# Kernel optimization log

Measured on AMD Instinct MI355X. Metric: run time of the kernel, lower is better.

## Reference

```python
import jax, jax.numpy as jnp
import numpy as np

B, S, T, C, Q = 8, 4096, 2048, 256, 256  # batch, ctx_steps, q_steps, context_size, query_size


def setup_inputs() -> dict:
    key = jax.random.key(0)
    k1, k2, k3, k4 = jax.random.split(key, 4)
    context = jax.random.normal(k1, (B, S, C), dtype=jnp.float32)
    query = jax.random.normal(k2, (T, B, Q), dtype=jnp.float32)
    context_mask = jax.random.randint(k3, (B, S), 0, 2).astype(bool)  # True = masked
    W = jax.random.normal(k4, (C, Q), dtype=jnp.float32)  # bilinear weights [context_size, query_size]
    return {"context": context, "query": query, "context_mask": context_mask, "W": W}


def reference(context, query, context_mask, W):
    # temp = 'auto' -> sqrt(query_size)
    temp = jnp.asarray(np.sqrt(Q), dtype=context.dtype)
    # scores[b,t,s] = (context[b,s,:] @ W) . query[t,b,:]
    scores = jnp.einsum('bsc,cq,tbq->bts', context, W, query) / temp
    neg = jnp.finfo(scores.dtype).min
    scores = jnp.where(context_mask[:, None, :], neg, scores)  # mask over ctx_steps
    attn = jax.nn.softmax(scores, axis=2)  # [B, T, S]
    # rows whose entire context is masked -> attention zeroed
    all_masked = jnp.all(context_mask, axis=1)[:, None, None]
    attn = jnp.where(all_masked, jnp.zeros((), attn.dtype), attn)
    composition = jnp.einsum('bts,bsc->btc', attn, context)  # [B, T, C]
    # module returns (attn, composition) permuted to [T, B, ...]
    return attn.transpose(1, 0, 2), composition.transpose(1, 0, 2)
```

## Files before the change

kernel.cpp:

```cpp
#include <hip/hip_runtime.h>

#define B_ 8
#define S_ 4096
#define T_ 2048
#define C_ 256
#define Q_ 256
#define NROW (T_ * B_)

typedef _Float16 f16;
typedef _Float16 f16x8 __attribute__((ext_vector_type(8)));
typedef _Float16 f16x4 __attribute__((ext_vector_type(4)));
typedef _Float16 f16x2 __attribute__((ext_vector_type(2)));
typedef float f32x4 __attribute__((ext_vector_type(4)));

#define MFMA(a, b, c) __builtin_amdgcn_mfma_f32_16x16x32_f16((a), (b), (c), 0, 0, 0)

__global__ void k_mask_mode(const unsigned char* __restrict__ mb, int* __restrict__ mode,
                            int* __restrict__ allm) {
  __shared__ int s0_, s123_;
  if (threadIdx.x == 0) { s0_ = 0; s123_ = 0; }
  __syncthreads();
  int a0 = 0, a123 = 0;
  int base = threadIdx.x * 128;
  for (int i = 0; i < 128; ++i) {
    int idx = base + i;
    int v = mb[idx];
    if (idx & 3) a123 |= v; else a0 |= v;
  }
  if (a0) atomicOr(&s0_, 1);
  if (a123) atomicOr(&s123_, 1);
  __syncthreads();
  if (threadIdx.x == 0) {
    int m;
    if (s123_ == 0 && s0_ == 0) m = 3;
    else if (s123_ == 0) m = 0;
    else if (s0_ == 0) m = 2;
    else m = 1;
    *mode = m;
  }
  if (threadIdx.x < B_) allm[threadIdx.x] = 1;
}

__global__ void k_expand_mask(const void* __restrict__ mp, const int* __restrict__ mode,
                              float* __restrict__ maskf, int* __restrict__ allm) {
  int i = blockIdx.x * 256 + threadIdx.x;
  int md = *mode;
  int m;
  if (md == 0)      m = ((const int*)mp)[i] != 0;
  else if (md == 1) m = ((const unsigned char*)mp)[i] != 0;
  else if (md == 2) m = ((const float*)mp)[i] != 0.0f;
  else              m = 0;
  maskf[i] = m ? 1.0f : 0.0f;
  if (!m) atomicAnd(&allm[i / S_], 0);
}

__global__ void k_conv_w(const float* __restrict__ W, f16* __restrict__ WT) {
  int i = blockIdx.x * 256 + threadIdx.x;
  int c = i >> 8, q = i & 255;
  WT[q * C_ + c] = (f16)W[i];
}

__global__ void k_conv_q(const float* __restrict__ q, f16* __restrict__ qT) {
  int i = blockIdx.x * 256 + threadIdx.x;
  int e = i * 4;
  int t = e / (B_ * Q_);
  int rb = e - t * (B_ * Q_);
  int b = rb >> 8;
  int qq = rb & 255;
  f32x4 v = *(const f32x4*)(q + e);
  f16x4 h; h[0] = (f16)v[0]; h[1] = (f16)v[1]; h[2] = (f16)v[2]; h[3] = (f16)v[3];
  *(f16x4*)(qT + ((size_t)(b * T_ + t)) * Q_ + qq) = h;
}

__global__ void k_transpose_ctx(const float* __restrict__ ctx, f16* __restrict__ ctxT) {
  __shared__ f16 tile[64][65];
  int s0 = blockIdx.x * 64, c0 = blockIdx.y * 64, b = blockIdx.z;
  int r = threadIdx.x >> 2;
  int cs = (threadIdx.x & 3) * 16;
  const float* src = ctx + ((size_t)(b * S_ + s0 + r)) * C_ + c0 + cs;
  f32x4 v0 = ((const f32x4*)src)[0];
  f32x4 v1 = ((const f32x4*)src)[1];
  f32x4 v2 = ((const f32x4*)src)[2];
  f32x4 v3 = ((const f32x4*)src)[3];
#pragma unroll
  for (int j = 0; j < 4; ++j) {
    tile[r][cs + j] = (f16)v0[j];
    tile[r][cs + 4 + j] = (f16)v1[j];
    tile[r][cs + 8 + j] = (f16)v2[j];
    tile[r][cs + 12 + j] = (f16)v3[j];
  }
  __syncthreads();
  int c = threadIdx.x >> 2;
  int ss = (threadIdx.x & 3) * 16;
  f16x8 o0, o1;
#pragma unroll
  for (int j = 0; j < 8; ++j) { o0[j] = tile[ss + j][c]; o1[j] = tile[ss + 8 + j][c]; }
  f16* dst = ctxT + ((size_t)(b * C_ + c0 + c)) * S_ + s0 + ss;
  *(f16x8*)dst = o0;
  *(f16x8*)(dst + 8) = o1;
}

__launch_bounds__(256, 2)
__global__ void k_gemm_cw(const float* __restrict__ ctx, const f16* __restrict__ WT,
                          f16* __restrict__ CW) {
  __shared__ alignas(16) f16 As[128 * 32];
  __shared__ alignas(16) f16 Bs[128 * 32];
  int n0 = blockIdx.x * 128;
  int m0 = blockIdx.y * 128;
  int tid = threadIdx.x;
  int w = tid >> 6, l = tid & 63;
  int wm = (w >> 1) * 64, wn = (w & 1) * 64;
  int lr = l & 15, lk = (l >> 4) * 8;
  f32x4 acc[4][4] = {};
  for (int k0 = 0; k0 < C_; k0 += 32) {
    __syncthreads();
#pragma unroll
    for (int it = 0; it < 2; ++it) {
      int h = (it * 256 + tid) * 8;
      int row = h >> 5, kk = h & 31;
      const float* ap = ctx + (size_t)(m0 + row) * C_ + k0 + kk;
      f32x4 x0 = ((const f32x4*)ap)[0];
      f32x4 x1 = ((const f32x4*)ap)[1];
      f16x8 hv;
#pragma unroll
      for (int j = 0; j < 4; ++j) { hv[j] = (f16)x0[j]; hv[4 + j] = (f16)x1[j]; }
      *(f16x8*)&As[row * 32 + kk] = hv;
    }
#pragma unroll
    for (int it = 0; it < 2; ++it) {
      int h = (it * 256 + tid) * 8;
      int row = h >> 5, kk = h & 31;
      *(f16x8*)&Bs[row * 32 + kk] = *(const f16x8*)&WT[(size_t)(n0 + row) * C_ + k0 + kk];
    }
    __syncthreads();
    f16x8 af[4], bf[4];
#pragma unroll
    for (int m = 0; m < 4; ++m) af[m] = *(const f16x8*)&As[(wm + m * 16 + lr) * 32 + lk];
#pragma unroll
    for (int n = 0; n < 4; ++n) bf[n] = *(const f16x8*)&Bs[(wn + n * 16 + lr) * 32 + lk];
#pragma unroll
    for (int m = 0; m < 4; ++m)
#pragma unroll
      for (int n = 0; n < 4; ++n) acc[m][n] = MFMA(af[m], bf[n], acc[m][n]);
  }
#pragma unroll
  for (int m = 0; m < 4; ++m)
#pragma unroll
    for (int n = 0; n < 4; ++n)
#pragma unroll
      for (int i = 0; i < 4; ++i) {
        int gm = m0 + wm + m * 16 + (l >> 4) * 4 + i;
        int gn = n0 + wn + n * 16 + lr;
        CW[(size_t)gm * Q_ + gn] = (f16)(acc[m][n][i] * 0.0625f);
      }
}

__launch_bounds__(256, 2)
__global__ void k_gemm_scores(const f16* __restrict__ qT, const f16* __restrict__ CW,
                              const float* __restrict__ maskf, float* __restrict__ attn,
                              float* __restrict__ pmax, float* __restrict__ psum) {
  __shared__ alignas(16) f16 As[128 * 32];
  __shared__ alignas(16) f16 Bs[128 * 32];
  int n0 = blockIdx.x * 128;
  int m0 = blockIdx.y * 128;
  int b = blockIdx.z;
  const f16* A = qT + (size_t)b * T_ * Q_;
  const f16* Bm = CW + (size_t)b * S_ * Q_;
  int tid = threadIdx.x;
  int w = tid >> 6, l = tid & 63;
  int wm = (w >> 1) * 64, wn = (w & 1) * 64;
  int lr = l & 15, lk = (l >> 4) * 8;
  f32x4 acc[4][4] = {};
  for (int k0 = 0; k0 < Q_; k0 += 32) {
    __syncthreads();
#pragma unroll
    for (int it = 0; it < 2; ++it) {
      int h = (it * 256 + tid) * 8;
      int row = h >> 5, kk = h & 31;
      *(f16x8*)&As[row * 32 + kk] = *(const f16x8*)&A[(size_t)(m0 + row) * Q_ + k0 + kk];
    }
#pragma unroll
    for (int it = 0; it < 2; ++it) {
      int h = (it * 256 + tid) * 8;
      int row = h >> 5, kk = h & 31;
      *(f16x8*)&Bs[row * 32 + kk] = *(const f16x8*)&Bm[(size_t)(n0 + row) * Q_ + k0 + kk];
    }
    __syncthreads();
    f16x8 af[4], bf[4];
#pragma unroll
    for (int m = 0; m < 4; ++m) af[m] = *(const f16x8*)&As[(wm + m * 16 + lr) * 32 + lk];
#pragma unroll
    for (int n = 0; n < 4; ++n) bf[n] = *(const f16x8*)&Bs[(wn + n * 16 + lr) * 32 + lk];
#pragma unroll
    for (int m = 0; m < 4; ++m)
#pragma unroll
      for (int n = 0; n < 4; ++n) acc[m][n] = MFMA(af[m], bf[n], acc[m][n]);
  }
  float msk[4];
#pragma unroll
  for (int n = 0; n < 4; ++n) msk[n] = maskf[b * S_ + n0 + wn + n * 16 + lr];
#pragma unroll
  for (int m = 0; m < 4; ++m)
#pragma unroll
    for (int n = 0; n < 4; ++n) {
      int gn = n0 + wn + n * 16 + lr;
#pragma unroll
      for (int i = 0; i < 4; ++i) {
        int gt = m0 + wm + m * 16 + (l >> 4) * 4 + i;
        float v = acc[m][n][i];
        if (msk[n] != 0.0f) v = -3.4e38f;
        acc[m][n][i] = v;
        attn[((size_t)gt * B_ + b) * S_ + gn] = v;
      }
    }
  int g = l >> 4;
  int ch = blockIdx.x * 2 + (w & 1);
#pragma unroll
  for (int m = 0; m < 4; ++m)
#pragma unroll
    for (int i = 0; i < 4; ++i) {
      float mx = fmaxf(fmaxf(acc[m][0][i], acc[m][1][i]), fmaxf(acc[m][2][i], acc[m][3][i]));
      mx = fmaxf(mx, __shfl_xor(mx, 1));
      mx = fmaxf(mx, __shfl_xor(mx, 2));
      mx = fmaxf(mx, __shfl_xor(mx, 4));
      mx = fmaxf(mx, __shfl_xor(mx, 8));
      float sm = 0.0f;
#pragma unroll
      for (int n = 0; n < 4; ++n) sm += __expf(acc[m][n][i] - mx);
      sm += __shfl_xor(sm, 1);
      sm += __shfl_xor(sm, 2);
      sm += __shfl_xor(sm, 4);
      sm += __shfl_xor(sm, 8);
      if (lr == 0) {
        int gt = m0 + wm + m * 16 + g * 4 + i;
        int r = gt * B_ + b;
        pmax[ch * NROW + r] = mx;
        psum[ch * NROW + r] = sm;
      }
    }
}

__launch_bounds__(256, 2)
__global__ void k_gemm_stats(const f16* __restrict__ qT, const f16* __restrict__ CW,
                             const float* __restrict__ maskf,
                             float* __restrict__ pmax, float* __restrict__ psum) {
  __shared__ alignas(16) f16 As[128 * 32];
  __shared__ alignas(16) f16 Bs[128 * 32];
  int n0 = blockIdx.x * 128;
  int m0 = blockIdx.y * 128;
  int b = blockIdx.z;
  const f16* A = qT + (size_t)b * T_ * Q_;
  const f16* Bm = CW + (size_t)b * S_ * Q_;
  int tid = threadIdx.x;
  int w = tid >> 6, l = tid & 63;
  int wm = (w >> 1) * 64, wn = (w & 1) * 64;
  int lr = l & 15, lk = (l >> 4) * 8;
  f32x4 acc[4][4] = {};
  for (int k0 = 0; k0 < Q_; k0 += 32) {
    __syncthreads();
#pragma unroll
    for (int it = 0; it < 2; ++it) {
      int h = (it * 256 + tid) * 8;
      int row = h >> 5, kk = h & 31;
      *(f16x8*)&As[row * 32 + kk] = *(const f16x8*)&A[(size_t)(m0 + row) * Q_ + k0 + kk];
    }
#pragma unroll
    for (int it = 0; it < 2; ++it) {
      int h = (it * 256 + tid) * 8;
      int row = h >> 5, kk = h & 31;
      *(f16x8*)&Bs[row * 32 + kk] = *(const f16x8*)&Bm[(size_t)(n0 + row) * Q_ + k0 + kk];
    }
    __syncthreads();
    f16x8 af[4], bf[4];
#pragma unroll
    for (int m = 0; m < 4; ++m) af[m] = *(const f16x8*)&As[(wm + m * 16 + lr) * 32 + lk];
#pragma unroll
    for (int n = 0; n < 4; ++n) bf[n] = *(const f16x8*)&Bs[(wn + n * 16 + lr) * 32 + lk];
#pragma unroll
    for (int m = 0; m < 4; ++m)
#pragma unroll
      for (int n = 0; n < 4; ++n) acc[m][n] = MFMA(af[m], bf[n], acc[m][n]);
  }
  float msk[4];
#pragma unroll
  for (int n = 0; n < 4; ++n) msk[n] = maskf[b * S_ + n0 + wn + n * 16 + lr];
#pragma unroll
  for (int m = 0; m < 4; ++m)
#pragma unroll
    for (int n = 0; n < 4; ++n) {
      if (msk[n] != 0.0f) {
#pragma unroll
        for (int i = 0; i < 4; ++i) acc[m][n][i] = -3.4e38f;
      }
    }
  int g = l >> 4;
  int ch = blockIdx.x * 2 + (w & 1);
#pragma unroll
  for (int m = 0; m < 4; ++m)
#pragma unroll
    for (int i = 0; i < 4; ++i) {
      float mx = fmaxf(fmaxf(acc[m][0][i], acc[m][1][i]), fmaxf(acc[m][2][i], acc[m][3][i]));
      mx = fmaxf(mx, __shfl_xor(mx, 1));
      mx = fmaxf(mx, __shfl_xor(mx, 2));
      mx = fmaxf(mx, __shfl_xor(mx, 4));
      mx = fmaxf(mx, __shfl_xor(mx, 8));
      float sm = 0.0f;
#pragma unroll
      for (int n = 0; n < 4; ++n) sm += __expf(acc[m][n][i] - mx);
      sm += __shfl_xor(sm, 1);
      sm += __shfl_xor(sm, 2);
      sm += __shfl_xor(sm, 4);
      sm += __shfl_xor(sm, 8);
      if (lr == 0) {
        int gt = m0 + wm + m * 16 + g * 4 + i;
        int r = gt * B_ + b;
        pmax[ch * NROW + r] = mx;
        psum[ch * NROW + r] = sm;
      }
    }
}

__global__ void k_finalize(const float* __restrict__ pmax, const float* __restrict__ psum,
                           float* __restrict__ rmax, float* __restrict__ rsum) {
  int r = blockIdx.x * 256 + threadIdx.x;
  float mx = -3.4e38f;
#pragma unroll 8
  for (int c = 0; c < 64; ++c) mx = fmaxf(mx, pmax[c * NROW + r]);
  float s = 0.0f;
#pragma unroll 8
  for (int c = 0; c < 64; ++c) s += psum[c * NROW + r] * __expf(pmax[c * NROW + r] - mx);
  rmax[r] = mx;
  rsum[r] = s;
}

__launch_bounds__(256, 2)
__global__ void k_comp(float* __restrict__ attn, const f16* __restrict__ ctxT,
                       const float* __restrict__ rmax, const float* __restrict__ rsum,
                       const int* __restrict__ allm, float* __restrict__ comp) {
  __shared__ alignas(16) f16 As[2][32 * 64];
  __shared__ alignas(16) f16 Bs[2][256 * 64];
  const int t0 = blockIdx.x * 32;
  const int b = blockIdx.y;
  const int tid = threadIdx.x;
  const int w = tid >> 6, l = tid & 63;
  const int lr = l & 15, hi = l >> 4;
  const int am = allm[b];
  const int ar = tid >> 4;
  const int cg = tid & 15;
  float mx0, mx1, inv0, inv1;
  float* aP0;
  float* aP1;
  {
    int r0 = (t0 + ar) * B_ + b;
    int r1 = (t0 + 16 + ar) * B_ + b;
    mx0 = rmax[r0]; mx1 = rmax[r1];
    inv0 = am ? 0.0f : (1.0f / rsum[r0]);
    inv1 = am ? 0.0f : (1.0f / rsum[r1]);
    aP0 = attn + (size_t)r0 * S_ + cg * 4;
    aP1 = attn + (size_t)r1 * S_ + cg * 4;
  }
  const int aswz = (cg * 8) ^ ((ar & 7) << 4);
  const int bc = tid >> 3;
  const int bs = tid & 7;
  const f16* bP = ctxT + ((size_t)(b * C_ + bc)) * S_ + bs * 8;
  const int bswz = (bs * 16) ^ ((bc & 7) << 4);
  f32x4 acc[2][4] = {};
  f32x4 aC0 = *(const f32x4*)aP0;
  f32x4 aC1 = *(const f32x4*)aP1;
  f16x8 bC[8];
#pragma unroll
  for (int i = 0; i < 8; ++i) bC[i] = *(const f16x8*)(bP + (size_t)i * 32 * S_);
  for (int k = 0; k < S_ / 64; ++k) {
    const int cur = k & 1;
    const int kn = (k + 1) * 64;
    f32x4 aN0 = *(const f32x4*)(aP0 + kn);
    f32x4 aN1 = *(const f32x4*)(aP1 + kn);
    f16x8 bN[8];
#pragma unroll
    for (int i = 0; i < 8; ++i) bN[i] = *(const f16x8*)(bP + (size_t)i * 32 * S_ + kn);
    f32x4 p0, p1;
#pragma unroll
    for (int e = 0; e < 4; ++e) {
      p0[e] = __expf(aC0[e] - mx0) * inv0;
      p1[e] = __expf(aC1[e] - mx1) * inv1;
    }
    *(f32x4*)(aP0 + k * 64) = p0;
    *(f32x4*)(aP1 + k * 64) = p1;
    f16x4 h0, h1;
#pragma unroll
    for (int e = 0; e < 4; ++e) { h0[e] = (f16)p0[e]; h1[e] = (f16)p1[e]; }
    *(f16x4*)((char*)As[cur] + ar * 128 + aswz) = h0;
    *(f16x4*)((char*)As[cur] + (16 + ar) * 128 + aswz) = h1;
#pragma unroll
    for (int i = 0; i < 8; ++i)
      *(f16x8*)((char*)Bs[cur] + (i * 32 + bc) * 128 + bswz) = bC[i];
    asm volatile("s_waitcnt lgkmcnt(0)" ::: "memory");
    __builtin_amdgcn_s_barrier();
    __builtin_amdgcn_sched_barrier(0);
#pragma unroll
    for (int kk = 0; kk < 2; ++kk) {
      const int cb = (kk * 64 + hi * 16) ^ ((lr & 7) << 4);
      f16x8 af[2], bf[4];
#pragma unroll
      for (int m = 0; m < 2; ++m)
        af[m] = *(const f16x8*)((char*)As[cur] + (m * 16 + lr) * 128 + cb);
#pragma unroll
      for (int n = 0; n < 4; ++n)
        bf[n] = *(const f16x8*)((char*)Bs[cur] + (w * 64 + n * 16 + lr) * 128 + cb);
#pragma unroll
      for (int m = 0; m < 2; ++m)
#pragma unroll
        for (int n = 0; n < 4; ++n) acc[m][n] = MFMA(af[m], bf[n], acc[m][n]);
    }
    aC0 = aN0; aC1 = aN1;
#pragma unroll
    for (int i = 0; i < 8; ++i) bC[i] = bN[i];
  }
#pragma unroll
  for (int m = 0; m < 2; ++m)
#pragma unroll
    for (int n = 0; n < 4; ++n)
#pragma unroll
      for (int i = 0; i < 4; ++i) {
        int tl = m * 16 + hi * 4 + i;
        int cc = w * 64 + n * 16 + lr;
        comp[((size_t)(t0 + tl) * B_ + b) * C_ + cc] = acc[m][n][i];
      }
}

__launch_bounds__(512, 1)
__global__ void k_fused4(const f16* __restrict__ qT, const f16* __restrict__ CW,
                         const f16* __restrict__ ctxT, const float* __restrict__ maskf,
                         const float* __restrict__ rmax, const float* __restrict__ rsum,
                         const int* __restrict__ allm,
                         float* __restrict__ attn, float* __restrict__ cptr) {
  __shared__ alignas(16) f16 Qs[128 * 256];
  __shared__ alignas(16) f16 Ps[2][128 * 64];
  __shared__ float2 Sm[128];
  const int CH = 32;
  const int bid = blockIdx.x;
  const int b = bid & 7;
  const int u = bid >> 3;
  const int t0 = (u & 15) * 128;
  const int sp = u >> 4;
  const int sbase = sp * (S_ / 2);
  const int tid = threadIdx.x;
  const int w = tid >> 6, l = tid & 63;
  const int lr = l & 15, hi = l >> 4;
  const int rswz = (lr & 7) << 4;
  const int wsg = (w & 3) * 16;
  const int wtg = (w >> 2) * 4;
  const int srow = wsg + lr;
  {
    const int qr = tid & 127;
    const int cb0 = (tid >> 7) * 128;
    const char* src = (const char*)(qT + ((size_t)(b * T_ + t0 + qr)) * Q_) + cb0;
#pragma unroll
    for (int j = 0; j < 8; ++j) {
      f16x8 v = *(const f16x8*)(src + j * 16);
      *(f16x8*)((char*)Qs + qr * 512 + ((cb0 + j * 16) ^ ((qr & 7) << 4))) = v;
    }
    if (tid < 128) {
      int r = (t0 + tid) * B_ + b;
      float2 sv;
      sv.x = rmax[r];
      sv.y = allm[b] ? 0.0f : (1.0f / rsum[r]);
      Sm[tid] = sv;
    }
  }
  const f16* cwL = CW + ((size_t)b * S_ + sbase + srow) * Q_ + hi * 8;
  const f16* cxL = ctxT + (size_t)(b * C_ + w * 32 + lr) * S_ + sbase + hi * 8;
  const float* maskP = maskf + b * S_ + sbase + srow;
  f32x4 accC[8][2] = {};
  __syncthreads();
  {
    float mk = maskP[0];
    f32x4 accS[4] = {};
#pragma unroll
    for (int g = 0; g < 2; ++g) {
      f16x8 cw4[4];
#pragma unroll
      for (int j = 0; j < 4; ++j)
        cw4[j] = *(const f16x8*)(cwL + (g * 4 + j) * 32);
#pragma unroll
      for (int j = 0; j < 4; ++j) {
        const int kq = g * 4 + j;
#pragma unroll
        for (int m = 0; m < 4; ++m) {
          f16x8 a = *(const f16x8*)((char*)Qs + ((wtg + m) * 16 + lr) * 512 +
                                    ((kq * 64 + hi * 16) ^ rswz));
          accS[m] = MFMA(a, cw4[j], accS[m]);
        }
      }
    }
#pragma unroll
    for (int m = 0; m < 4; ++m)
#pragma unroll
      for (int i = 0; i < 4; ++i) {
        int tl = (wtg + m) * 16 + hi * 4 + i;
        float2 sv = Sm[tl];
        float p = (mk != 0.0f) ? 0.0f : __expf(accS[m][i] - sv.x) * sv.y;
        float po = __shfl_xor(p, 1);
        if (!(lr & 1)) {
          float2 fp; fp.x = p; fp.y = po;
          *(float2*)&attn[((size_t)(t0 + tl) * B_ + b) * S_ + sbase + srow] = fp;
          f16x2 h; h[0] = (f16)p; h[1] = (f16)po;
          *(f16x2*)((char*)Ps[0] + ((tl * 128 + srow * 2) ^ ((tl & 7) << 4))) = h;
        }
      }
    asm volatile("s_waitcnt lgkmcnt(0)" ::: "memory");
    __builtin_amdgcn_s_barrier();
  }
  for (int k = 1; k < CH; ++k) {
    const int s0 = k * 64;
    const int sc0 = s0 - 64;
    const int cur = k & 1, prev = cur ^ 1;
    float mk = maskP[s0];
    f16x8 cx4[4];
#pragma unroll
    for (int kk = 0; kk < 2; ++kk)
#pragma unroll
      for (int n = 0; n < 2; ++n)
        cx4[kk * 2 + n] = *(const f16x8*)(cxL + (size_t)(n * 16) * S_ + sc0 + kk * 32);
    f32x4 accS[4] = {};
#pragma unroll
    for (int g = 0; g < 2; ++g) {
      f16x8 cw4[4];
#pragma unroll
      for (int j = 0; j < 4; ++j)
        cw4[j] = *(const f16x8*)(cwL + (size_t)s0 * Q_ + (g * 4 + j) * 32);
#pragma unroll
      for (int j = 0; j < 4; ++j) {
        const int kq = g * 4 + j;
#pragma unroll
        for (int m = 0; m < 4; ++m) {
          f16x8 a = *(const f16x8*)((char*)Qs + ((wtg + m) * 16 + lr) * 512 +
                                    ((kq * 64 + hi * 16) ^ rswz));
          accS[m] = MFMA(a, cw4[j], accS[m]);
        }
      }
    }
#pragma unroll
    for (int m = 0; m < 4; ++m)
#pragma unroll
      for (int i = 0; i < 4; ++i) {
        int tl = (wtg + m) * 16 + hi * 4 + i;
        float2 sv = Sm[tl];
        float p = (mk != 0.0f) ? 0.0f : __expf(accS[m][i] - sv.x) * sv.y;
        float po = __shfl_xor(p, 1);
        if (!(lr & 1)) {
          float2 fp; fp.x = p; fp.y = po;
          *(float2*)&attn[((size_t)(t0 + tl) * B_ + b) * S_ + sbase + s0 + srow] = fp;
          f16x2 h; h[0] = (f16)p; h[1] = (f16)po;
          *(f16x2*)((char*)Ps[cur] + ((tl * 128 + srow * 2) ^ ((tl & 7) << 4))) = h;
        }
      }
#pragma unroll
    for (int kk = 0; kk < 2; ++kk) {
#pragma unroll
      for (int m = 0; m < 8; ++m) {
        f16x8 pa = *(const f16x8*)((char*)Ps[prev] +
                                   (((m * 16 + lr) * 128 + kk * 64 + hi * 16) ^ rswz));
#pragma unroll
        for (int n = 0; n < 2; ++n) accC[m][n] = MFMA(pa, cx4[kk * 2 + n], accC[m][n]);
      }
    }
    asm volatile("s_waitcnt lgkmcnt(0)" ::: "memory");
    __builtin_amdgcn_s_barrier();
  }
  {
    const int sc0 = (CH - 1) * 64;
    const int prev = (CH - 1) & 1;
#pragma unroll
    for (int kk = 0; kk < 2; ++kk) {
      f16x8 cx2[2];
#pragma unroll
      for (int n = 0; n < 2; ++n)
        cx2[n] = *(const f16x8*)(cxL + (size_t)(n * 16) * S_ + sc0 + kk * 32);
#pragma unroll
      for (int m = 0; m < 8; ++m) {
        f16x8 pa = *(const f16x8*)((char*)Ps[prev] +
                                   (((m * 16 + lr) * 128 + kk * 64 + hi * 16) ^ rswz));
#pragma unroll
        for (int n = 0; n < 2; ++n) accC[m][n] = MFMA(pa, cx2[n], accC[m][n]);
      }
    }
  }
  float* cout = cptr + (size_t)sp * T_ * B_ * C_;
#pragma unroll
  for (int m = 0; m < 8; ++m)
#pragma unroll
    for (int n = 0; n < 2; ++n)
#pragma unroll
      for (int i = 0; i < 4; ++i) {
        int tl = m * 16 + hi * 4 + i;
        int cc = w * 32 + n * 16 + lr;
        cout[((size_t)(t0 + tl) * B_ + b) * C_ + cc] = accC[m][n][i];
      }
}

__global__ void k_comp_red(const float* __restrict__ P, float* __restrict__ comp) {
  size_t i = ((size_t)blockIdx.x * 256 + threadIdx.x) * 4;
  f32x4 a = *(const f32x4*)(P + i);
  f32x4 c = *(const f32x4*)(P + (size_t)T_ * B_ * C_ + i);
  f32x4 r;
#pragma unroll
  for (int e = 0; e < 4; ++e) r[e] = a[e] + c[e];
  *(f32x4*)(comp + i) = r;
}

extern "C" void kernel_launch(void* const* d_in, const int* in_sizes, int n_in,
                              void* d_out, int out_size, void* d_ws, size_t ws_size,
                              hipStream_t stream) {
  const float* ctx = (const float*)d_in[0];
  const float* query = (const float*)d_in[1];
  const void* mask = d_in[2];
  const float* W = (const float*)d_in[3];

  float* out = (float*)d_out;
  float* attn = out;
  float* comp = out + (size_t)T_ * B_ * S_;

  char* ws = (char*)d_ws;
  f16* ctxT = (f16*)(ws);
  f16* qT = (f16*)(ws + 16777216);
  f16* WT = (f16*)(ws + 25165824);
  float* maskf = (float*)(ws + 25296896);
  float* rmax = (float*)(ws + 25427968);
  float* rsum = (float*)(ws + 25493504);
  int* allm = (int*)(ws + 25559040);
  int* mode = (int*)(ws + 25559072);
  float* pmax = (float*)(ws + 25559168);
  float* psum = (float*)(ws + 29753472);

  k_mask_mode<<<1, 256, 0, stream>>>((const unsigned char*)mask, mode, allm);
  k_expand_mask<<<(B_ * S_) / 256, 256, 0, stream>>>(mask, mode, maskf, allm);
  k_conv_w<<<(C_ * Q_) / 256, 256, 0, stream>>>(W, WT);
  k_conv_q<<<(T_ * B_ * Q_ / 4) / 256, 256, 0, stream>>>(query, qT);
  k_transpose_ctx<<<dim3(S_ / 64, C_ / 64, B_), 256, 0, stream>>>(ctx, ctxT);

  if (ws_size >= (size_t)84279424) {
    f16* CW2 = (f16*)(ws + 33947776);
    float* compP = (float*)(ws + 50724992);
    k_gemm_cw<<<dim3(Q_ / 128, (B_ * S_) / 128), 256, 0, stream>>>(ctx, WT, CW2);
    k_gemm_stats<<<dim3(S_ / 128, T_ / 128, B_), 256, 0, stream>>>(qT, CW2, maskf, pmax, psum);
    k_finalize<<<NROW / 256, 256, 0, stream>>>(pmax, psum, rmax, rsum);
    k_fused4<<<dim3((T_ / 128) * B_ * 2), 512, 0, stream>>>(qT, CW2, ctxT, maskf, rmax, rsum,
                                                            allm, attn, compP);
    k_comp_red<<<(T_ * B_ * C_ / 4) / 256, 256, 0, stream>>>(compP, comp);
  } else {
    f16* CW = (f16*)comp;
    k_gemm_cw<<<dim3(Q_ / 128, (B_ * S_) / 128), 256, 0, stream>>>(ctx, WT, CW);
    k_gemm_scores<<<dim3(S_ / 128, T_ / 128, B_), 256, 0, stream>>>(qT, CW, maskf, attn, pmax, psum);
    k_finalize<<<NROW / 256, 256, 0, stream>>>(pmax, psum, rmax, rsum);
    k_comp<<<dim3(T_ / 32, B_), 256, 0, stream>>>(attn, ctxT, rmax, rsum, allm, comp);
  }
}
```

Measured before the change: 507.2 us.

## Prefetch next CW tile in fused kernel and use direct global-to-LDS loads in stats GEMM

```diff
diff --git a/kernel.cpp b/kernel.cpp
--- a/kernel.cpp
+++ b/kernel.cpp
@@ -14,6 +14,11 @@
 typedef float f32x4 __attribute__((ext_vector_type(4)));
 
 #define MFMA(a, b, c) __builtin_amdgcn_mfma_f32_16x16x32_f16((a), (b), (c), 0, 0, 0)
+
+typedef const __attribute__((address_space(1))) void* gas1_t;
+typedef __attribute__((address_space(3))) void* las3_t;
+#define GLDS16(gp, lp) \
+  __builtin_amdgcn_global_load_lds((gas1_t)(const void*)(gp), (las3_t)(void*)(lp), 16, 0, 0)
 
 __global__ void k_mask_mode(const unsigned char* __restrict__ mb, int* __restrict__ mode,
                             int* __restrict__ allm) {
@@ -241,9 +246,9 @@
 }
 
 __launch_bounds__(256, 2)
-__global__ void k_gemm_stats(const f16* __restrict__ qT, const f16* __restrict__ CW,
-                             const float* __restrict__ maskf,
-                             float* __restrict__ pmax, float* __restrict__ psum) {
+__global__ void k_gemm_stats2(const f16* __restrict__ qT, const f16* __restrict__ CW,
+                              const float* __restrict__ maskf,
+                              float* __restrict__ pmax, float* __restrict__ psum) {
   __shared__ alignas(16) f16 As[128 * 32];
   __shared__ alignas(16) f16 Bs[128 * 32];
   int n0 = blockIdx.x * 128;
@@ -255,20 +260,16 @@
   int w = tid >> 6, l = tid & 63;
   int wm = (w >> 1) * 64, wn = (w & 1) * 64;
   int lr = l & 15, lk = (l >> 4) * 8;
+  int srw = l >> 2;
+  int scl = (l & 3) * 8;
   f32x4 acc[4][4] = {};
   for (int k0 = 0; k0 < Q_; k0 += 32) {
     __syncthreads();
 #pragma unroll
     for (int it = 0; it < 2; ++it) {
-      int h = (it * 256 + tid) * 8;
-      int row = h >> 5, kk = h & 31;
-      *(f16x8*)&As[row * 32 + kk] = *(const f16x8*)&A[(size_t)(m0 + row) * Q_ + k0 + kk];
-    }
-#pragma unroll
-    for (int it = 0; it < 2; ++it) {
-      int h = (it * 256 + tid) * 8;
-      int row = h >> 5, kk = h & 31;
-      *(f16x8*)&Bs[row * 32 + kk] = *(const f16x8*)&Bm[(size_t)(n0 + row) * Q_ + k0 + kk];
+      int rb = w * 32 + it * 16;
+      GLDS16(A + (size_t)(m0 + rb + srw) * Q_ + k0 + scl, (char*)As + rb * 64);
+      GLDS16(Bm + (size_t)(n0 + rb + srw) * Q_ + k0 + scl, (char*)Bs + rb * 64);
     }
     __syncthreads();
     f16x8 af[4], bf[4];
@@ -429,7 +430,7 @@
 }
 
 __launch_bounds__(512, 1)
-__global__ void k_fused4(const f16* __restrict__ qT, const f16* __restrict__ CW,
+__global__ void k_fused5(const f16* __restrict__ qT, const f16* __restrict__ CW,
                          const f16* __restrict__ ctxT, const float* __restrict__ maskf,
                          const float* __restrict__ rmax, const float* __restrict__ rsum,
                          const int* __restrict__ allm,
@@ -472,25 +473,35 @@
   const f16* cxL = ctxT + (size_t)(b * C_ + w * 32 + lr) * S_ + sbase + hi * 8;
   const float* maskP = maskf + b * S_ + sbase + srow;
   f32x4 accC[8][2] = {};
+  f16x8 cwA[8], cwB[8];
+  float mkA = maskP[0], mkB = 0.0f;
+#pragma unroll
+  for (int j = 0; j < 8; ++j) cwA[j] = *(const f16x8*)(cwL + j * 32);
   __syncthreads();
-  {
-    float mk = maskP[0];
+  auto ITER = [&](int k, f16x8(&CWC)[8], f16x8(&CWN)[8], float mkc, float& mkn) {
+    const int s0 = k * 64;
+    const int sc0 = s0 - 64;
+    const int cur = k & 1, prev = cur ^ 1;
+    f16x8 cx4[4];
+#pragma unroll
+    for (int kk = 0; kk < 2; ++kk)
+#pragma unroll
+      for (int n = 0; n < 2; ++n)
+        cx4[kk * 2 + n] = *(const f16x8*)(cxL + (size_t)(n * 16) * S_ + sc0 + kk * 32);
+    if (k < CH - 1) {
+#pragma unroll
+      for (int j = 0; j < 8; ++j)
+        CWN[j] = *(const f16x8*)(cwL + (size_t)(s0 + 64) * Q_ + j * 32);
+      mkn = maskP[s0 + 64];
+    }
     f32x4 accS[4] = {};
 #pragma unroll
-    for (int g = 0; g < 2; ++g) {
-      f16x8 cw4[4];
-#pragma unroll
-      for (int j = 0; j < 4; ++j)
-        cw4[j] = *(const f16x8*)(cwL + (g * 4 + j) * 32);
-#pragma unroll
-      for (int j = 0; j < 4; ++j) {
-        const int kq = g * 4 + j;
-#pragma unroll
-        for (int m = 0; m < 4; ++m) {
-          f16x8 a = *(const f16x8*)((char*)Qs + ((wtg + m) * 16 + lr) * 512 +
-                                    ((kq * 64 + hi * 16) ^ rswz));
-          accS[m] = MFMA(a, cw4[j], accS[m]);
-        }
+    for (int j = 0; j < 8; ++j) {
+#pragma unroll
+      for (int m = 0; m < 4; ++m) {
+        f16x8 a = *(const f16x8*)((char*)Qs + ((wtg + m) * 16 + lr) * 512 +
+                                  ((j * 64 + hi * 16) ^ rswz));
+        accS[m] = MFMA(a, CWC[j], accS[m]);
       }
     }
 #pragma unroll
@@ -499,7 +510,49 @@
       for (int i = 0; i < 4; ++i) {
         int tl = (wtg + m) * 16 + hi * 4 + i;
         float2 sv = Sm[tl];
-        float p = (mk != 0.0f) ? 0.0f : __expf(accS[m][i] - sv.x) * sv.y;
+        float p = (mkc != 0.0f) ? 0.0f : __expf(accS[m][i] - sv.x) * sv.y;
+        float po = __shfl_xor(p, 1);
+        if (!(lr & 1)) {
+          float2 fp; fp.x = p; fp.y = po;
+          *(float2*)&attn[((size_t)(t0 + tl) * B_ + b) * S_ + sbase + s0 + srow] = fp;
+          f16x2 h; h[0] = (f16)p; h[1] = (f16)po;
+          *(f16x2*)((char*)Ps[cur] + ((tl * 128 + srow * 2) ^ ((tl & 7) << 4))) = h;
+        }
+      }
+#pragma unroll
+    for (int kk = 0; kk < 2; ++kk) {
+#pragma unroll
+      for (int m = 0; m < 8; ++m) {
+        f16x8 pa = *(const f16x8*)((char*)Ps[prev] +
+                                   (((m * 16 + lr) * 128 + kk * 64 + hi * 16) ^ rswz));
+#pragma unroll
+        for (int n = 0; n < 2; ++n) accC[m][n] = MFMA(pa, cx4[kk * 2 + n], accC[m][n]);
+      }
+    }
+    asm volatile("s_waitcnt lgkmcnt(0)" ::: "memory");
+    __builtin_amdgcn_s_barrier();
+  };
+  {
+#pragma unroll
+    for (int j = 0; j < 8; ++j) cwB[j] = *(const f16x8*)(cwL + (size_t)64 * Q_ + j * 32);
+    mkB = maskP[64];
+    f32x4 accS[4] = {};
+#pragma unroll
+    for (int j = 0; j < 8; ++j) {
+#pragma unroll
+      for (int m = 0; m < 4; ++m) {
+        f16x8 a = *(const f16x8*)((char*)Qs + ((wtg + m) * 16 + lr) * 512 +
+                                  ((j * 64 + hi * 16) ^ rswz));
+        accS[m] = MFMA(a, cwA[j], accS[m]);
+      }
+    }
+#pragma unroll
+    for (int m = 0; m < 4; ++m)
+#pragma unroll
+      for (int i = 0; i < 4; ++i) {
+        int tl = (wtg + m) * 16 + hi * 4 + i;
+        float2 sv = Sm[tl];
+        float p = (mkA != 0.0f) ? 0.0f : __expf(accS[m][i] - sv.x) * sv.y;
         float po = __shfl_xor(p, 1);
         if (!(lr & 1)) {
           float2 fp; fp.x = p; fp.y = po;
@@ -511,63 +564,11 @@
     asm volatile("s_waitcnt lgkmcnt(0)" ::: "memory");
     __builtin_amdgcn_s_barrier();
   }
-  for (int k = 1; k < CH; ++k) {
-    const int s0 = k * 64;
-    const int sc0 = s0 - 64;
-    const int cur = k & 1, prev = cur ^ 1;
-    float mk = maskP[s0];
-    f16x8 cx4[4];
-#pragma unroll
-    for (int kk = 0; kk < 2; ++kk)
-#pragma unroll
-      for (int n = 0; n < 2; ++n)
-        cx4[kk * 2 + n] = *(const f16x8*)(cxL + (size_t)(n * 16) * S_ + sc0 + kk * 32);
-    f32x4 accS[4] = {};
-#pragma unroll
-    for (int g = 0; g < 2; ++g) {
-      f16x8 cw4[4];
-#pragma unroll
-      for (int j = 0; j < 4; ++j)
-        cw4[j] = *(const f16x8*)(cwL + (size_t)s0 * Q_ + (g * 4 + j) * 32);
-#pragma unroll
-      for (int j = 0; j < 4; ++j) {
-        const int kq = g * 4 + j;
-#pragma unroll
-        for (int m = 0; m < 4; ++m) {
-          f16x8 a = *(const f16x8*)((char*)Qs + ((wtg + m) * 16 + lr) * 512 +
-                                    ((kq * 64 + hi * 16) ^ rswz));
-          accS[m] = MFMA(a, cw4[j], accS[m]);
-        }
-      }
-    }
-#pragma unroll
-    for (int m = 0; m < 4; ++m)
-#pragma unroll
-      for (int i = 0; i < 4; ++i) {
-        int tl = (wtg + m) * 16 + hi * 4 + i;
-        float2 sv = Sm[tl];
-        float p = (mk != 0.0f) ? 0.0f : __expf(accS[m][i] - sv.x) * sv.y;
-        float po = __shfl_xor(p, 1);
-        if (!(lr & 1)) {
-          float2 fp; fp.x = p; fp.y = po;
-          *(float2*)&attn[((size_t)(t0 + tl) * B_ + b) * S_ + sbase + s0 + srow] = fp;
-          f16x2 h; h[0] = (f16)p; h[1] = (f16)po;
-          *(f16x2*)((char*)Ps[cur] + ((tl * 128 + srow * 2) ^ ((tl & 7) << 4))) = h;
-        }
-      }
-#pragma unroll
-    for (int kk = 0; kk < 2; ++kk) {
-#pragma unroll
-      for (int m = 0; m < 8; ++m) {
-        f16x8 pa = *(const f16x8*)((char*)Ps[prev] +
-                                   (((m * 16 + lr) * 128 + kk * 64 + hi * 16) ^ rswz));
-#pragma unroll
-        for (int n = 0; n < 2; ++n) accC[m][n] = MFMA(pa, cx4[kk * 2 + n], accC[m][n]);
-      }
-    }
-    asm volatile("s_waitcnt lgkmcnt(0)" ::: "memory");
-    __builtin_amdgcn_s_barrier();
-  }
+  for (int k = 1; k + 1 < CH; k += 2) {
+    ITER(k, cwB, cwA, mkB, mkA);
+    ITER(k + 1, cwA, cwB, mkA, mkB);
+  }
+  ITER(CH - 1, cwB, cwA, mkB, mkA);
   {
     const int sc0 = (CH - 1) * 64;
     const int prev = (CH - 1) & 1;
@@ -643,9 +644,9 @@
     f16* CW2 = (f16*)(ws + 33947776);
     float* compP = (float*)(ws + 50724992);
     k_gemm_cw<<<dim3(Q_ / 128, (B_ * S_) / 128), 256, 0, stream>>>(ctx, WT, CW2);
-    k_gemm_stats<<<dim3(S_ / 128, T_ / 128, B_), 256, 0, stream>>>(qT, CW2, maskf, pmax, psum);
+    k_gemm_stats2<<<dim3(S_ / 128, T_ / 128, B_), 256, 0, stream>>>(qT, CW2, maskf, pmax, psum);
     k_finalize<<<NROW / 256, 256, 0, stream>>>(pmax, psum, rmax, rsum);
-    k_fused4<<<dim3((T_ / 128) * B_ * 2), 512, 0, stream>>>(qT, CW2, ctxT, maskf, rmax, rsum,
+    k_fused5<<<dim3((T_ / 128) * B_ * 2), 512, 0, stream>>>(qT, CW2, ctxT, maskf, rmax, rsum,
                                                             allm, attn, compP);
     k_comp_red<<<(T_ * B_ * C_ / 4) / 256, 256, 0, stream>>>(compP, comp);
   } else {
```

New measurement: 523.3 us. +3.2%, slower.

## Rewrite stats GEMM with 256x256 tiles, double-buffered direct global-to-LDS loads

Applied to the files above, without the earlier changes.

```diff
diff --git a/kernel.cpp b/kernel.cpp
--- a/kernel.cpp
+++ b/kernel.cpp
@@ -14,6 +14,11 @@
 typedef float f32x4 __attribute__((ext_vector_type(4)));
 
 #define MFMA(a, b, c) __builtin_amdgcn_mfma_f32_16x16x32_f16((a), (b), (c), 0, 0, 0)
+
+typedef const __attribute__((address_space(1))) void* gas1_t;
+typedef __attribute__((address_space(3))) void* las3_t;
+#define GLDS16(gp, lp) \
+  __builtin_amdgcn_global_load_lds((gas1_t)(const void*)(gp), (las3_t)(void*)(lp), 16, 0, 0)
 
 __global__ void k_mask_mode(const unsigned char* __restrict__ mb, int* __restrict__ mode,
                             int* __restrict__ allm) {
@@ -240,52 +245,59 @@
     }
 }
 
-__launch_bounds__(256, 2)
-__global__ void k_gemm_stats(const f16* __restrict__ qT, const f16* __restrict__ CW,
-                             const float* __restrict__ maskf,
-                             float* __restrict__ pmax, float* __restrict__ psum) {
-  __shared__ alignas(16) f16 As[128 * 32];
-  __shared__ alignas(16) f16 Bs[128 * 32];
-  int n0 = blockIdx.x * 128;
-  int m0 = blockIdx.y * 128;
+__launch_bounds__(512, 1)
+__global__ void k_gemm_stats3(const f16* __restrict__ qT, const f16* __restrict__ CW,
+                              const float* __restrict__ maskf,
+                              float* __restrict__ pmax, float* __restrict__ psum) {
+  __shared__ alignas(16) f16 As[2][256 * 32];
+  __shared__ alignas(16) f16 Bs[2][256 * 32];
+  int n0 = blockIdx.x * 256;
+  int m0 = blockIdx.y * 256;
   int b = blockIdx.z;
   const f16* A = qT + (size_t)b * T_ * Q_;
   const f16* Bm = CW + (size_t)b * S_ * Q_;
   int tid = threadIdx.x;
   int w = tid >> 6, l = tid & 63;
-  int wm = (w >> 1) * 64, wn = (w & 1) * 64;
+  int wm = (w >> 2) * 128;
+  int wn = (w & 3) * 64;
   int lr = l & 15, lk = (l >> 4) * 8;
-  f32x4 acc[4][4] = {};
-  for (int k0 = 0; k0 < Q_; k0 += 32) {
+  int srw = l >> 2;
+  int scl = (l & 3) * 8;
+  f32x4 acc[8][4] = {};
+#pragma unroll
+  for (int it = 0; it < 2; ++it) {
+    int rb = w * 32 + it * 16;
+    GLDS16(A + (size_t)(m0 + rb + srw) * Q_ + scl, (char*)As[0] + rb * 64);
+    GLDS16(Bm + (size_t)(n0 + rb + srw) * Q_ + scl, (char*)Bs[0] + rb * 64);
+  }
+  __syncthreads();
+  for (int ks = 0; ks < 8; ++ks) {
+    int cur = ks & 1;
+    if (ks < 7) {
+      int k0 = (ks + 1) * 32;
+#pragma unroll
+      for (int it = 0; it < 2; ++it) {
+        int rb = w * 32 + it * 16;
+        GLDS16(A + (size_t)(m0 + rb + srw) * Q_ + k0 + scl, (char*)As[cur ^ 1] + rb * 64);
+        GLDS16(Bm + (size_t)(n0 + rb + srw) * Q_ + k0 + scl, (char*)Bs[cur ^ 1] + rb * 64);
+      }
+    }
+    f16x8 bf[4];
+#pragma unroll
+    for (int n = 0; n < 4; ++n) bf[n] = *(const f16x8*)&Bs[cur][(wn + n * 16 + lr) * 32 + lk];
+#pragma unroll
+    for (int m = 0; m < 8; ++m) {
+      f16x8 af = *(const f16x8*)&As[cur][(wm + m * 16 + lr) * 32 + lk];
+#pragma unroll
+      for (int n = 0; n < 4; ++n) acc[m][n] = MFMA(af, bf[n], acc[m][n]);
+    }
     __syncthreads();
-#pragma unroll
-    for (int it = 0; it < 2; ++it) {
-      int h = (it * 256 + tid) * 8;
-      int row = h >> 5, kk = h & 31;
-      *(f16x8*)&As[row * 32 + kk] = *(const f16x8*)&A[(size_t)(m0 + row) * Q_ + k0 + kk];
-    }
-#pragma unroll
-    for (int it = 0; it < 2; ++it) {
-      int h = (it * 256 + tid) * 8;
-      int row = h >> 5, kk = h & 31;
-      *(f16x8*)&Bs[row * 32 + kk] = *(const f16x8*)&Bm[(size_t)(n0 + row) * Q_ + k0 + kk];
-    }
-    __syncthreads();
-    f16x8 af[4], bf[4];
-#pragma unroll
-    for (int m = 0; m < 4; ++m) af[m] = *(const f16x8*)&As[(wm + m * 16 + lr) * 32 + lk];
-#pragma unroll
-    for (int n = 0; n < 4; ++n) bf[n] = *(const f16x8*)&Bs[(wn + n * 16 + lr) * 32 + lk];
-#pragma unroll
-    for (int m = 0; m < 4; ++m)
-#pragma unroll
-      for (int n = 0; n < 4; ++n) acc[m][n] = MFMA(af[m], bf[n], acc[m][n]);
   }
   float msk[4];
 #pragma unroll
   for (int n = 0; n < 4; ++n) msk[n] = maskf[b * S_ + n0 + wn + n * 16 + lr];
 #pragma unroll
-  for (int m = 0; m < 4; ++m)
+  for (int m = 0; m < 8; ++m)
 #pragma unroll
     for (int n = 0; n < 4; ++n) {
       if (msk[n] != 0.0f) {
@@ -294,9 +306,9 @@
       }
     }
   int g = l >> 4;
-  int ch = blockIdx.x * 2 + (w & 1);
-#pragma unroll
-  for (int m = 0; m < 4; ++m)
+  int ch = blockIdx.x * 4 + (w & 3);
+#pragma unroll
+  for (int m = 0; m < 8; ++m)
 #pragma unroll
     for (int i = 0; i < 4; ++i) {
       float mx = fmaxf(fmaxf(acc[m][0][i], acc[m][1][i]), fmaxf(acc[m][2][i], acc[m][3][i]));
@@ -643,7 +655,7 @@
     f16* CW2 = (f16*)(ws + 33947776);
     float* compP = (float*)(ws + 50724992);
     k_gemm_cw<<<dim3(Q_ / 128, (B_ * S_) / 128), 256, 0, stream>>>(ctx, WT, CW2);
-    k_gemm_stats<<<dim3(S_ / 128, T_ / 128, B_), 256, 0, stream>>>(qT, CW2, maskf, pmax, psum);
+    k_gemm_stats3<<<dim3(S_ / 256, T_ / 256, B_), 512, 0, stream>>>(qT, CW2, maskf, pmax, psum);
     k_finalize<<<NROW / 256, 256, 0, stream>>>(pmax, psum, rmax, rsum);
     k_fused4<<<dim3((T_ / 128) * B_ * 2), 512, 0, stream>>>(qT, CW2, ctxT, maskf, rmax, rsum,
                                                             allm, attn, compP);
```

After: 527.7 us. +4.0%, slower.

## Replace stats GEMM with Q-resident LDS kernel streaming CW chunks

Applied to the files above, without the earlier changes.

```diff
diff --git a/kernel.cpp b/kernel.cpp
--- a/kernel.cpp
+++ b/kernel.cpp
@@ -240,84 +240,110 @@
     }
 }
 
-__launch_bounds__(256, 2)
-__global__ void k_gemm_stats(const f16* __restrict__ qT, const f16* __restrict__ CW,
-                             const float* __restrict__ maskf,
-                             float* __restrict__ pmax, float* __restrict__ psum) {
-  __shared__ alignas(16) f16 As[128 * 32];
-  __shared__ alignas(16) f16 Bs[128 * 32];
-  int n0 = blockIdx.x * 128;
-  int m0 = blockIdx.y * 128;
-  int b = blockIdx.z;
-  const f16* A = qT + (size_t)b * T_ * Q_;
-  const f16* Bm = CW + (size_t)b * S_ * Q_;
-  int tid = threadIdx.x;
-  int w = tid >> 6, l = tid & 63;
-  int wm = (w >> 1) * 64, wn = (w & 1) * 64;
-  int lr = l & 15, lk = (l >> 4) * 8;
-  f32x4 acc[4][4] = {};
-  for (int k0 = 0; k0 < Q_; k0 += 32) {
+__launch_bounds__(512, 4)
+__global__ void k_stats4(const f16* __restrict__ qT, const f16* __restrict__ CW,
+                         const float* __restrict__ maskf,
+                         float* __restrict__ pmax, float* __restrict__ psum) {
+  __shared__ alignas(16) f16 Qs[128 * 256];
+  __shared__ alignas(16) float RedM[2][128][4];
+  __shared__ alignas(16) float RedS[2][128][4];
+  const int CH = 16;
+  const int bid = blockIdx.x;
+  const int b = bid & 7;
+  const int u = bid >> 3;
+  const int t0 = (u & 15) * 128;
+  const int sp = u >> 4;
+  const int sbase = sp * (S_ / 4);
+  const int tid = threadIdx.x;
+  const int w = tid >> 6, l = tid & 63;
+  const int lr = l & 15, hi = l >> 4;
+  const int rswz = (lr & 7) << 4;
+  const int wsg = (w & 3) * 16;
+  const int wtg = (w >> 2) * 4;
+  const int srow = wsg + lr;
+  {
+    const int qr = tid & 127;
+    const int cb0 = (tid >> 7) * 128;
+    const char* src = (const char*)(qT + ((size_t)(b * T_ + t0 + qr)) * Q_) + cb0;
+#pragma unroll
+    for (int j = 0; j < 8; ++j) {
+      f16x8 v = *(const f16x8*)(src + j * 16);
+      *(f16x8*)((char*)Qs + qr * 512 + ((cb0 + j * 16) ^ ((qr & 7) << 4))) = v;
+    }
+  }
+  const f16* cwL = CW + ((size_t)b * S_ + sbase + srow) * Q_ + hi * 8;
+  const float* maskP = maskf + b * S_ + sbase + srow;
+  __syncthreads();
+  for (int k = 0; k < CH; ++k) {
+    const int s0 = k * 64;
+    const int pk = k & 1;
+    float mk = maskP[s0];
+    f32x4 accS[4] = {};
+#pragma unroll
+    for (int g = 0; g < 2; ++g) {
+      f16x8 cw4[4];
+#pragma unroll
+      for (int j = 0; j < 4; ++j)
+        cw4[j] = *(const f16x8*)(cwL + (size_t)s0 * Q_ + (g * 4 + j) * 32);
+#pragma unroll
+      for (int j = 0; j < 4; ++j) {
+        const int kq = g * 4 + j;
+#pragma unroll
+        for (int m = 0; m < 4; ++m) {
+          f16x8 a = *(const f16x8*)((char*)Qs + ((wtg + m) * 16 + lr) * 512 +
+                                    ((kq * 64 + hi * 16) ^ rswz));
+          accS[m] = MFMA(a, cw4[j], accS[m]);
+        }
+      }
+    }
+    if (mk != 0.0f) {
+#pragma unroll
+      for (int m = 0; m < 4; ++m)
+#pragma unroll
+        for (int i = 0; i < 4; ++i) accS[m][i] = -3.4e38f;
+    }
+#pragma unroll
+    for (int m = 0; m < 4; ++m)
+#pragma unroll
+      for (int i = 0; i < 4; ++i) {
+        float v = accS[m][i];
+        v = fmaxf(v, __shfl_xor(v, 1));
+        v = fmaxf(v, __shfl_xor(v, 2));
+        v = fmaxf(v, __shfl_xor(v, 4));
+        v = fmaxf(v, __shfl_xor(v, 8));
+        if (lr == 0) RedM[pk][(wtg + m) * 16 + hi * 4 + i][w & 3] = v;
+      }
     __syncthreads();
 #pragma unroll
-    for (int it = 0; it < 2; ++it) {
-      int h = (it * 256 + tid) * 8;
-      int row = h >> 5, kk = h & 31;
-      *(f16x8*)&As[row * 32 + kk] = *(const f16x8*)&A[(size_t)(m0 + row) * Q_ + k0 + kk];
-    }
-#pragma unroll
-    for (int it = 0; it < 2; ++it) {
-      int h = (it * 256 + tid) * 8;
-      int row = h >> 5, kk = h & 31;
-      *(f16x8*)&Bs[row * 32 + kk] = *(const f16x8*)&Bm[(size_t)(n0 + row) * Q_ + k0 + kk];
-    }
+    for (int m = 0; m < 4; ++m)
+#pragma unroll
+      for (int i = 0; i < 4; ++i) {
+        int tl = (wtg + m) * 16 + hi * 4 + i;
+        float4 r4 = *(const float4*)&RedM[pk][tl][0];
+        float mx = fmaxf(fmaxf(r4.x, r4.y), fmaxf(r4.z, r4.w));
+        float e = __expf(accS[m][i] - mx);
+        e += __shfl_xor(e, 1);
+        e += __shfl_xor(e, 2);
+        e += __shfl_xor(e, 4);
+        e += __shfl_xor(e, 8);
+        if (lr == 0) RedS[pk][tl][w & 3] = e;
+      }
     __syncthreads();
-    f16x8 af[4], bf[4];
-#pragma unroll
-    for (int m = 0; m < 4; ++m) af[m] = *(const f16x8*)&As[(wm + m * 16 + lr) * 32 + lk];
-#pragma unroll
-    for (int n = 0; n < 4; ++n) bf[n] = *(const f16x8*)&Bs[(wn + n * 16 + lr) * 32 + lk];
-#pragma unroll
-    for (int m = 0; m < 4; ++m)
-#pragma unroll
-      for (int n = 0; n < 4; ++n) acc[m][n] = MFMA(af[m], bf[n], acc[m][n]);
-  }
-  float msk[4];
-#pragma unroll
-  for (int n = 0; n < 4; ++n) msk[n] = maskf[b * S_ + n0 + wn + n * 16 + lr];
-#pragma unroll
-  for (int m = 0; m < 4; ++m)
-#pragma unroll
-    for (int n = 0; n < 4; ++n) {
-      if (msk[n] != 0.0f) {
-#pragma unroll
-        for (int i = 0; i < 4; ++i) acc[m][n][i] = -3.4e38f;
-      }
-    }
-  int g = l >> 4;
-  int ch = blockIdx.x * 2 + (w & 1);
-#pragma unroll
-  for (int m = 0; m < 4; ++m)
-#pragma unroll
-    for (int i = 0; i < 4; ++i) {
-      float mx = fmaxf(fmaxf(acc[m][0][i], acc[m][1][i]), fmaxf(acc[m][2][i], acc[m][3][i]));
-      mx = fmaxf(mx, __shfl_xor(mx, 1));
-      mx = fmaxf(mx, __shfl_xor(mx, 2));
-      mx = fmaxf(mx, __shfl_xor(mx, 4));
-      mx = fmaxf(mx, __shfl_xor(mx, 8));
-      float sm = 0.0f;
-#pragma unroll
-      for (int n = 0; n < 4; ++n) sm += __expf(acc[m][n][i] - mx);
-      sm += __shfl_xor(sm, 1);
-      sm += __shfl_xor(sm, 2);
-      sm += __shfl_xor(sm, 4);
-      sm += __shfl_xor(sm, 8);
-      if (lr == 0) {
-        int gt = m0 + wm + m * 16 + g * 4 + i;
-        int r = gt * B_ + b;
-        pmax[ch * NROW + r] = mx;
-        psum[ch * NROW + r] = sm;
-      }
-    }
+    if ((w & 3) == 0 && lr == 0) {
+      int ch = sp * CH + k;
+#pragma unroll
+      for (int m = 0; m < 4; ++m)
+#pragma unroll
+        for (int i = 0; i < 4; ++i) {
+          int tl = (wtg + m) * 16 + hi * 4 + i;
+          float4 r4 = *(const float4*)&RedM[pk][tl][0];
+          float4 s4 = *(const float4*)&RedS[pk][tl][0];
+          int r = (t0 + tl) * B_ + b;
+          pmax[ch * NROW + r] = fmaxf(fmaxf(r4.x, r4.y), fmaxf(r4.z, r4.w));
+          psum[ch * NROW + r] = (s4.x + s4.y) + (s4.z + s4.w);
+        }
+    }
+  }
 }
 
 __global__ void k_finalize(const float* __restrict__ pmax, const float* __restrict__ psum,
@@ -643,7 +669,7 @@
     f16* CW2 = (f16*)(ws + 33947776);
     float* compP = (float*)(ws + 50724992);
     k_gemm_cw<<<dim3(Q_ / 128, (B_ * S_) / 128), 256, 0, stream>>>(ctx, WT, CW2);
-    k_gemm_stats<<<dim3(S_ / 128, T_ / 128, B_), 256, 0, stream>>>(qT, CW2, maskf, pmax, psum);
+    k_stats4<<<dim3(8 * 16 * 4), 512, 0, stream>>>(qT, CW2, maskf, pmax, psum);
     k_finalize<<<NROW / 256, 256, 0, stream>>>(pmax, psum, rmax, rsum);
     k_fused4<<<dim3((T_ / 128) * B_ * 2), 512, 0, stream>>>(qT, CW2, ctxT, maskf, rmax, rsum,
                                                             allm, attn, compP);
```

Result: slower. 617.0 us (+21.6%).
